# Kernel optimization log

Hardware: AMD Instinct MI355X
Metric: run time of the kernel (lower is better)

Reference implementation:

```python
import jax, jax.numpy as jnp
import numpy as np

N_NODES = 200000
N_EDGES = 6400000
IN_DIM = 15      # pfc_input_dim
POS_DIM = 4      # positional_dim
OUT_DIM = 2      # vtx_classes + 1


def setup_inputs() -> dict:
    key = jax.random.key(0)
    k1, k2, k3, k4, k5, k6, k7 = jax.random.split(key, 7)
    x_pfc = jax.random.normal(k1, (N_NODES, IN_DIM), dtype=jnp.float32)
    edge_index = jax.random.randint(k2, (2, N_EDGES), 0, N_NODES, dtype=jnp.int64)
    s_in = 1.0 / np.sqrt(IN_DIM)
    s_pos = 1.0 / np.sqrt(POS_DIM)
    # PointTransformerConv params: lin, lin_src, lin_dst (no bias), pos_nn = Linear(4, 2)
    W_lin = jax.random.uniform(k3, (OUT_DIM, IN_DIM), jnp.float32, -s_in, s_in)
    W_src = jax.random.uniform(k4, (OUT_DIM, IN_DIM), jnp.float32, -s_in, s_in)
    W_dst = jax.random.uniform(k5, (OUT_DIM, IN_DIM), jnp.float32, -s_in, s_in)
    W_pos = jax.random.uniform(k6, (OUT_DIM, POS_DIM), jnp.float32, -s_pos, s_pos)
    b_pos = jax.random.uniform(k7, (OUT_DIM,), jnp.float32, -s_pos, s_pos)
    return {"x_pfc": x_pfc, "edge_index": edge_index, "W_lin": W_lin,
            "W_src": W_src, "W_dst": W_dst, "W_pos": W_pos, "b_pos": b_pos}


def reference(x_pfc, edge_index, W_lin, W_src, W_dst, W_pos, b_pos):
    n = x_pfc.shape[0]
    pos = x_pfc[:, :POS_DIM]
    # original forward calls ptc_only(x, pos, edge_index.flip(0)):
    # source j = edge_index[1], target i = edge_index[0]
    j = edge_index[1]
    i = edge_index[0]
    # node-level linear maps (N x OUT_DIM)
    v = x_pfc @ W_lin.T
    a_src = x_pfc @ W_src.T
    a_dst = x_pfc @ W_dst.T
    # positional MLP on relative positions (E x OUT_DIM)
    delta = (pos[i] - pos[j]) @ W_pos.T + b_pos
    alpha = a_dst[i] - a_src[j] + delta
    # segment softmax over incoming edges of each target node i
    m = jax.ops.segment_max(alpha, i, num_segments=n)  # -inf for empty segments (never indexed)
    e = jnp.exp(alpha - m[i])
    denom = jax.ops.segment_sum(e, i, num_segments=n)
    attn = e / (denom[i] + 1e-16)
    msg = attn * (v[j] + delta)
    return jax.ops.segment_sum(msg, i, num_segments=n)
```

## Files before the change

### kernel.cpp

```cpp
#include <hip/hip_runtime.h>

#define N_NODES 200000
#define N_EDGES 6400000
#define IN_DIM 15
#define POS_DIM 4

#define CSHIFT 9
#define CMASK 511
#define CW 512
#define NCOARSE ((N_NODES + CW - 1) >> CSHIFT)
#define CHUNK 16384
#define NBLK ((N_EDGES + CHUNK - 1) / CHUNK)
#define CAP 17408
#define SUB 8192

typedef unsigned uv4 __attribute__((ext_vector_type(4)));


__global__ void node_prep(const float* __restrict__ x,
                          const float* __restrict__ Wlin,
                          const float* __restrict__ Wsrc,
                          const float* __restrict__ Wpos,
                          float4* __restrict__ tabJ,
                          unsigned* __restrict__ gcnt)
{
    int n = blockIdx.x * blockDim.x + threadIdx.x;
    if (n < NCOARSE) gcnt[n] = 0u;
    if (n >= N_NODES) return;
    const float* xp = x + (long)n * IN_DIM;
    float xv[IN_DIM];
#pragma unroll
    for (int k = 0; k < IN_DIM; ++k) xv[k] = xp[k];

    float p0 = 0.f, p1 = 0.f;
#pragma unroll
    for (int k = 0; k < POS_DIM; ++k) {
        p0 += Wpos[k] * xv[k];
        p1 += Wpos[POS_DIM + k] * xv[k];
    }
    float v0 = 0.f, v1 = 0.f, as0 = 0.f, as1 = 0.f;
#pragma unroll
    for (int k = 0; k < IN_DIM; ++k) {
        float xk = xv[k];
        v0  += Wlin[k] * xk;  v1  += Wlin[IN_DIM + k] * xk;
        as0 += Wsrc[k] * xk;  as1 += Wsrc[IN_DIM + k] * xk;
    }
    tabJ[n] = make_float4(as0 + p0, as1 + p1, v0 - p0, v1 - p1);
}

__global__ void scatter_kernel(const int* __restrict__ idx,
                               unsigned* __restrict__ gcnt,
                               unsigned* __restrict__ packed)
{
    __shared__ unsigned stage[CHUNK];
    __shared__ unsigned cnt[512];
    __shared__ unsigned sc[512];
    __shared__ unsigned lloc[512];
    __shared__ unsigned gdst[NCOARSE];
    int b = blockIdx.x;
    int t = threadIdx.x;
    long s0 = (long)b * CHUNK;
    int end = (int)min((long)CHUNK, (long)N_EDGES - s0);
    cnt[t] = 0u;
    __syncthreads();
    for (int e = t * 4; e < end; e += 2048) {
        int4 iv = *(const int4*)(idx + s0 + e);
        atomicAdd(&cnt[iv.x >> CSHIFT], 1u);
        atomicAdd(&cnt[iv.y >> CSHIFT], 1u);
        atomicAdd(&cnt[iv.z >> CSHIFT], 1u);
        atomicAdd(&cnt[iv.w >> CSHIFT], 1u);
    }
    __syncthreads();
    sc[t] = cnt[t];
    __syncthreads();
    for (int o = 1; o < 512; o <<= 1) {
        unsigned a = (t >= o) ? sc[t - o] : 0u;
        __syncthreads();
        sc[t] += a;
        __syncthreads();
    }
    {
        unsigned c  = cnt[t];
        unsigned ex = sc[t] - c;
        lloc[t] = ex;
        if (t < NCOARSE) gdst[t] = atomicAdd(&gcnt[t], c);
        cnt[t] = ex;
    }
    __syncthreads();
    for (int e = t * 4; e < end; e += 2048) {
        int4 iv = *(const int4*)(idx + s0 + e);
        int4 jv = *(const int4*)(idx + N_EDGES + s0 + e);
        unsigned r0 = atomicAdd(&cnt[iv.x >> CSHIFT], 1u);
        unsigned r1 = atomicAdd(&cnt[iv.y >> CSHIFT], 1u);
        unsigned r2 = atomicAdd(&cnt[iv.z >> CSHIFT], 1u);
        unsigned r3 = atomicAdd(&cnt[iv.w >> CSHIFT], 1u);
        stage[r0] = ((unsigned)jv.x << CSHIFT) | (unsigned)(iv.x & CMASK);
        stage[r1] = ((unsigned)jv.y << CSHIFT) | (unsigned)(iv.y & CMASK);
        stage[r2] = ((unsigned)jv.z << CSHIFT) | (unsigned)(iv.z & CMASK);
        stage[r3] = ((unsigned)jv.w << CSHIFT) | (unsigned)(iv.w & CMASK);
    }
    __syncthreads();
    int wid = t >> 6, lane = t & 63;
    for (int bk = wid; bk < NCOARSE; bk += 8) {
        unsigned st  = lloc[bk];
        unsigned len = lloc[bk + 1] - st;
        unsigned gb  = gdst[bk];
        unsigned rem = (gb < (unsigned)CAP) ? (unsigned)CAP - gb : 0u;
        if (len > rem) len = rem;
        unsigned* dst = packed + (size_t)bk * CAP + gb;
        for (unsigned e = lane; e < len; e += 64u)
            dst[e] = stage[st + e];
    }
}

__global__ __launch_bounds__(512, 8) void
bucket_agg_kernel(const unsigned* __restrict__ packed,
                  const unsigned* __restrict__ gcnt,
                  const float* __restrict__ x,
                  const float* __restrict__ Wdst,
                  const float* __restrict__ Wpos,
                  const float4* __restrict__ tabJ,
                  const float* __restrict__ bpos,
                  float2* __restrict__ out)
{
    __shared__ unsigned cache[SUB + 512];
    __shared__ unsigned cnt[512], sc[512], cur[512];
    int k = blockIdx.x;
    int t = threadIdx.x;
    float b0 = bpos[0], b1 = bpos[1];
    int gn = (k << CSHIFT) + t;

    float p0 = 0.f, p1 = 0.f, ad0 = 0.f, ad1 = 0.f;
    if (gn < N_NODES) {
        const float* xp = x + (long)gn * IN_DIM;
        float xv[IN_DIM];
#pragma unroll
        for (int q = 0; q < IN_DIM; ++q) xv[q] = xp[q];
#pragma unroll
        for (int q = 0; q < POS_DIM; ++q) {
            p0 += Wpos[q] * xv[q];
            p1 += Wpos[POS_DIM + q] * xv[q];
        }
#pragma unroll
        for (int q = 0; q < IN_DIM; ++q) {
            ad0 += Wdst[q] * xv[q];
            ad1 += Wdst[IN_DIM + q] * xv[q];
        }
    }
    float a0 = ad0 + p0 + b0, a1 = ad1 + p1 + b1;
    float sn0 = 0.f, sn1 = 0.f, sd0 = 0.f, sd1 = 0.f;

    unsigned n = min(gcnt[k], (unsigned)CAP);
    const unsigned* pk = packed + (size_t)k * CAP;

    for (unsigned c0 = 0; c0 < n; c0 += SUB) {
        unsigned m = min(n - c0, (unsigned)SUB);
        cnt[t] = 0u;
        __syncthreads();
        for (unsigned e = 4u * t; e < m; e += 2048u) {
            uv4 p = *(const uv4*)(pk + c0 + e);
            atomicAdd(&cnt[p.x & CMASK], 1u);
            if (e + 1 < m) atomicAdd(&cnt[p.y & CMASK], 1u);
            if (e + 2 < m) atomicAdd(&cnt[p.z & CMASK], 1u);
            if (e + 3 < m) atomicAdd(&cnt[p.w & CMASK], 1u);
        }
        __syncthreads();
        sc[t] = cnt[t];
        __syncthreads();
        for (int o = 1; o < 512; o <<= 1) {
            unsigned a = (t >= o) ? sc[t - o] : 0u;
            __syncthreads();
            sc[t] += a;
            __syncthreads();
        }
        unsigned deg = cnt[t];
        unsigned st  = sc[t] - deg + (unsigned)t;
        cur[t] = st;
        __syncthreads();
        for (unsigned e = 4u * t; e < m; e += 2048u) {
            uv4 p = *(const uv4*)(pk + c0 + e);
            { unsigned pos = atomicAdd(&cur[p.x & CMASK], 1u); cache[pos] = p.x >> CSHIFT; }
            if (e + 1 < m) { unsigned pos = atomicAdd(&cur[p.y & CMASK], 1u); cache[pos] = p.y >> CSHIFT; }
            if (e + 2 < m) { unsigned pos = atomicAdd(&cur[p.z & CMASK], 1u); cache[pos] = p.z >> CSHIFT; }
            if (e + 3 < m) { unsigned pos = atomicAdd(&cur[p.w & CMASK], 1u); cache[pos] = p.w >> CSHIFT; }
        }
        __syncthreads();
        unsigned e = 0;
        for (; e + 4u <= deg; e += 4u) {
            unsigned j0 = cache[st + e],     j1 = cache[st + e + 1];
            unsigned j2 = cache[st + e + 2], j3 = cache[st + e + 3];
            float4 f0 = tabJ[j0], f1 = tabJ[j1], f2 = tabJ[j2], f3 = tabJ[j3];
            float e00 = __expf(a0 - f0.x), e01 = __expf(a1 - f0.y);
            float e10 = __expf(a0 - f1.x), e11 = __expf(a1 - f1.y);
            float e20 = __expf(a0 - f2.x), e21 = __expf(a1 - f2.y);
            float e30 = __expf(a0 - f3.x), e31 = __expf(a1 - f3.y);
            sn0 += e00 * f0.z + e10 * f1.z + e20 * f2.z + e30 * f3.z;
            sn1 += e01 * f0.w + e11 * f1.w + e21 * f2.w + e31 * f3.w;
            sd0 += e00 + e10 + e20 + e30;
            sd1 += e01 + e11 + e21 + e31;
        }
        for (; e < deg; ++e) {
            unsigned j = cache[st + e];
            float4 fj = tabJ[j];
            float e0 = __expf(a0 - fj.x), e1 = __expf(a1 - fj.y);
            sn0 += e0 * fj.z;  sn1 += e1 * fj.w;
            sd0 += e0;         sd1 += e1;
        }
    }

    if (gn >= N_NODES) return;
    float o0 = (sn0 + (p0 + b0) * sd0) / (sd0 + 1e-16f);
    float o1 = (sn1 + (p1 + b1) * sd1) / (sd1 + 1e-16f);
    out[gn] = make_float2(o0, o1);
}

extern "C" void kernel_launch(void* const* d_in, const int* in_sizes, int n_in,
                              void* d_out, int out_size, void* d_ws, size_t ws_size,
                              hipStream_t stream) {
    const float* x    = (const float*)d_in[0];
    const int*   idx  = (const int*)d_in[1];
    const float* Wlin = (const float*)d_in[2];
    const float* Wsrc = (const float*)d_in[3];
    const float* Wdst = (const float*)d_in[4];
    const float* Wpos = (const float*)d_in[5];
    const float* bpos = (const float*)d_in[6];
    float* out = (float*)d_out;

    char* ws = (char*)d_ws;
    size_t off = 0;
    float4* tabJ = (float4*)(ws + off); off += (size_t)N_NODES * 16;
    unsigned* packed = (unsigned*)(ws + off); off += (size_t)NCOARSE * CAP * 4;
    unsigned* gcnt   = (unsigned*)(ws + off); off += (size_t)NCOARSE * 4;

    node_prep<<<(N_NODES + 255) / 256, 256, 0, stream>>>(x, Wlin, Wsrc, Wpos,
                                                         tabJ, gcnt);
    scatter_kernel<<<NBLK, 512, 0, stream>>>(idx, gcnt, packed);
    bucket_agg_kernel<<<NCOARSE, 512, 0, stream>>>(packed, gcnt,
                                                   x, Wdst, Wpos, tabJ, bpos,
                                                   (float2*)out);
}
```

Before: 169.8 us.

## Split each coarse bucket across two blocks and use wave-shuffle scans

The aggregation kernel now launches two 256-thread blocks per 512-node bucket. Each block reads the whole bucket but keeps only edges whose target falls in its half, which removes the SUB-chunk loop and doubles the number of blocks. Both kernels replace the shared-memory Hillis-Steele scan, with its many barriers, by a wave-level shuffle scan plus a small cross-wave sum. The gather loop is unrolled to 8 and the second pass over packed edges uses nontemporal loads. The cost is that every packed edge is read twice from global memory, once per half-block. Per-half capacity HCAP assumes balanced halves, and overflow past HCAP is unchecked.

Measured after the change: 172.6 us. About the same (+1.6%).

```diff
diff --git a/kernel.cpp b/kernel.cpp
--- a/kernel.cpp
+++ b/kernel.cpp
@@ -12,7 +12,7 @@
 #define CHUNK 16384
 #define NBLK ((N_EDGES + CHUNK - 1) / CHUNK)
 #define CAP 17408
-#define SUB 8192
+#define HCAP 8704
 
 typedef unsigned uv4 __attribute__((ext_vector_type(4)));
 
@@ -54,11 +54,12 @@
 {
     __shared__ unsigned stage[CHUNK];
     __shared__ unsigned cnt[512];
-    __shared__ unsigned sc[512];
     __shared__ unsigned lloc[512];
     __shared__ unsigned gdst[NCOARSE];
+    __shared__ unsigned wsum[8];
     int b = blockIdx.x;
     int t = threadIdx.x;
+    int lane = t & 63, wid = t >> 6;
     long s0 = (long)b * CHUNK;
     int end = (int)min((long)CHUNK, (long)N_EDGES - s0);
     cnt[t] = 0u;
@@ -71,20 +72,23 @@
         atomicAdd(&cnt[iv.w >> CSHIFT], 1u);
     }
     __syncthreads();
-    sc[t] = cnt[t];
-    __syncthreads();
-    for (int o = 1; o < 512; o <<= 1) {
-        unsigned a = (t >= o) ? sc[t - o] : 0u;
-        __syncthreads();
-        sc[t] += a;
-        __syncthreads();
-    }
+    unsigned v = cnt[t];
+    unsigned s = v;
+#pragma unroll
+    for (int off = 1; off < 64; off <<= 1) {
+        unsigned u = __shfl_up(s, off, 64);
+        if (lane >= off) s += u;
+    }
+    if (lane == 63) wsum[wid] = s;
+    __syncthreads();
+    unsigned woff = 0;
+#pragma unroll
+    for (int w = 0; w < 8; ++w) woff += (w < wid) ? wsum[w] : 0u;
     {
-        unsigned c  = cnt[t];
-        unsigned ex = sc[t] - c;
+        unsigned ex = woff + s - v;
         lloc[t] = ex;
-        if (t < NCOARSE) gdst[t] = atomicAdd(&gcnt[t], c);
         cnt[t] = ex;
+        if (t < NCOARSE) gdst[t] = atomicAdd(&gcnt[t], v);
     }
     __syncthreads();
     for (int e = t * 4; e < end; e += 2048) {
@@ -100,7 +104,6 @@
         stage[r3] = ((unsigned)jv.w << CSHIFT) | (unsigned)(iv.w & CMASK);
     }
     __syncthreads();
-    int wid = t >> 6, lane = t & 63;
     for (int bk = wid; bk < NCOARSE; bk += 8) {
         unsigned st  = lloc[bk];
         unsigned len = lloc[bk + 1] - st;
@@ -113,7 +116,7 @@
     }
 }
 
-__global__ __launch_bounds__(512, 8) void
+__global__ __launch_bounds__(256) void
 bucket_agg_kernel(const unsigned* __restrict__ packed,
                   const unsigned* __restrict__ gcnt,
                   const float* __restrict__ x,
@@ -123,12 +126,16 @@
                   const float* __restrict__ bpos,
                   float2* __restrict__ out)
 {
-    __shared__ unsigned cache[SUB + 512];
-    __shared__ unsigned cnt[512], sc[512], cur[512];
-    int k = blockIdx.x;
+    __shared__ unsigned cache[HCAP + 512];
+    __shared__ unsigned cnt[256], cur[256];
+    __shared__ unsigned wsum[4];
+    int blk = blockIdx.x;
+    int k = blk >> 1;
+    unsigned half = (unsigned)(blk & 1);
     int t = threadIdx.x;
+    int lane = t & 63, wid = t >> 6;
     float b0 = bpos[0], b1 = bpos[1];
-    int gn = (k << CSHIFT) + t;
+    int gn = (k << CSHIFT) + ((int)half << 8) + t;
 
     float p0 = 0.f, p1 = 0.f, ad0 = 0.f, ad1 = 0.f;
     if (gn < N_NODES) {
@@ -153,59 +160,71 @@
     unsigned n = min(gcnt[k], (unsigned)CAP);
     const unsigned* pk = packed + (size_t)k * CAP;
 
-    for (unsigned c0 = 0; c0 < n; c0 += SUB) {
-        unsigned m = min(n - c0, (unsigned)SUB);
-        cnt[t] = 0u;
-        __syncthreads();
-        for (unsigned e = 4u * t; e < m; e += 2048u) {
-            uv4 p = *(const uv4*)(pk + c0 + e);
-            atomicAdd(&cnt[p.x & CMASK], 1u);
-            if (e + 1 < m) atomicAdd(&cnt[p.y & CMASK], 1u);
-            if (e + 2 < m) atomicAdd(&cnt[p.z & CMASK], 1u);
-            if (e + 3 < m) atomicAdd(&cnt[p.w & CMASK], 1u);
-        }
-        __syncthreads();
-        sc[t] = cnt[t];
-        __syncthreads();
-        for (int o = 1; o < 512; o <<= 1) {
-            unsigned a = (t >= o) ? sc[t - o] : 0u;
-            __syncthreads();
-            sc[t] += a;
-            __syncthreads();
-        }
-        unsigned deg = cnt[t];
-        unsigned st  = sc[t] - deg + (unsigned)t;
-        cur[t] = st;
-        __syncthreads();
-        for (unsigned e = 4u * t; e < m; e += 2048u) {
-            uv4 p = *(const uv4*)(pk + c0 + e);
-            { unsigned pos = atomicAdd(&cur[p.x & CMASK], 1u); cache[pos] = p.x >> CSHIFT; }
-            if (e + 1 < m) { unsigned pos = atomicAdd(&cur[p.y & CMASK], 1u); cache[pos] = p.y >> CSHIFT; }
-            if (e + 2 < m) { unsigned pos = atomicAdd(&cur[p.z & CMASK], 1u); cache[pos] = p.z >> CSHIFT; }
-            if (e + 3 < m) { unsigned pos = atomicAdd(&cur[p.w & CMASK], 1u); cache[pos] = p.w >> CSHIFT; }
-        }
-        __syncthreads();
-        unsigned e = 0;
-        for (; e + 4u <= deg; e += 4u) {
-            unsigned j0 = cache[st + e],     j1 = cache[st + e + 1];
-            unsigned j2 = cache[st + e + 2], j3 = cache[st + e + 3];
-            float4 f0 = tabJ[j0], f1 = tabJ[j1], f2 = tabJ[j2], f3 = tabJ[j3];
-            float e00 = __expf(a0 - f0.x), e01 = __expf(a1 - f0.y);
-            float e10 = __expf(a0 - f1.x), e11 = __expf(a1 - f1.y);
-            float e20 = __expf(a0 - f2.x), e21 = __expf(a1 - f2.y);
-            float e30 = __expf(a0 - f3.x), e31 = __expf(a1 - f3.y);
-            sn0 += e00 * f0.z + e10 * f1.z + e20 * f2.z + e30 * f3.z;
-            sn1 += e01 * f0.w + e11 * f1.w + e21 * f2.w + e31 * f3.w;
-            sd0 += e00 + e10 + e20 + e30;
-            sd1 += e01 + e11 + e21 + e31;
-        }
-        for (; e < deg; ++e) {
-            unsigned j = cache[st + e];
-            float4 fj = tabJ[j];
-            float e0 = __expf(a0 - fj.x), e1 = __expf(a1 - fj.y);
-            sn0 += e0 * fj.z;  sn1 += e1 * fj.w;
-            sd0 += e0;         sd1 += e1;
-        }
+#define KEEP(w) ((((w) & CMASK) >> 8) == half)
+    cnt[t] = 0u;
+    __syncthreads();
+    for (unsigned e = 4u * t; e < n; e += 1024u) {
+        uv4 p = *(const uv4*)(pk + e);
+        if (KEEP(p.x))               atomicAdd(&cnt[p.x & 255u], 1u);
+        if (e + 1 < n && KEEP(p.y))  atomicAdd(&cnt[p.y & 255u], 1u);
+        if (e + 2 < n && KEEP(p.z))  atomicAdd(&cnt[p.z & 255u], 1u);
+        if (e + 3 < n && KEEP(p.w))  atomicAdd(&cnt[p.w & 255u], 1u);
+    }
+    __syncthreads();
+    unsigned v = cnt[t];
+    unsigned s = v;
+#pragma unroll
+    for (int off = 1; off < 64; off <<= 1) {
+        unsigned u = __shfl_up(s, off, 64);
+        if (lane >= off) s += u;
+    }
+    if (lane == 63) wsum[wid] = s;
+    __syncthreads();
+    unsigned woff = 0;
+#pragma unroll
+    for (int w = 0; w < 4; ++w) woff += (w < wid) ? wsum[w] : 0u;
+    unsigned deg = v;
+    unsigned st  = woff + s - v + (unsigned)t;
+    cur[t] = st;
+    __syncthreads();
+    for (unsigned e = 4u * t; e < n; e += 1024u) {
+        uv4 p = __builtin_nontemporal_load((const uv4*)(pk + e));
+        if (KEEP(p.x))              { unsigned pos = atomicAdd(&cur[p.x & 255u], 1u); cache[pos] = p.x >> CSHIFT; }
+        if (e + 1 < n && KEEP(p.y)) { unsigned pos = atomicAdd(&cur[p.y & 255u], 1u); cache[pos] = p.y >> CSHIFT; }
+        if (e + 2 < n && KEEP(p.z)) { unsigned pos = atomicAdd(&cur[p.z & 255u], 1u); cache[pos] = p.z >> CSHIFT; }
+        if (e + 3 < n && KEEP(p.w)) { unsigned pos = atomicAdd(&cur[p.w & 255u], 1u); cache[pos] = p.w >> CSHIFT; }
+    }
+#undef KEEP
+    __syncthreads();
+    unsigned e = 0;
+    for (; e + 8u <= deg; e += 8u) {
+        unsigned j0 = cache[st + e],     j1 = cache[st + e + 1];
+        unsigned j2 = cache[st + e + 2], j3 = cache[st + e + 3];
+        unsigned j4 = cache[st + e + 4], j5 = cache[st + e + 5];
+        unsigned j6 = cache[st + e + 6], j7 = cache[st + e + 7];
+        float4 f0 = tabJ[j0], f1 = tabJ[j1], f2 = tabJ[j2], f3 = tabJ[j3];
+        float4 f4 = tabJ[j4], f5 = tabJ[j5], f6 = tabJ[j6], f7 = tabJ[j7];
+        float e00 = __expf(a0 - f0.x), e01 = __expf(a1 - f0.y);
+        float e10 = __expf(a0 - f1.x), e11 = __expf(a1 - f1.y);
+        float e20 = __expf(a0 - f2.x), e21 = __expf(a1 - f2.y);
+        float e30 = __expf(a0 - f3.x), e31 = __expf(a1 - f3.y);
+        float e40 = __expf(a0 - f4.x), e41 = __expf(a1 - f4.y);
+        float e50 = __expf(a0 - f5.x), e51 = __expf(a1 - f5.y);
+        float e60 = __expf(a0 - f6.x), e61 = __expf(a1 - f6.y);
+        float e70 = __expf(a0 - f7.x), e71 = __expf(a1 - f7.y);
+        sn0 += e00 * f0.z + e10 * f1.z + e20 * f2.z + e30 * f3.z
+             + e40 * f4.z + e50 * f5.z + e60 * f6.z + e70 * f7.z;
+        sn1 += e01 * f0.w + e11 * f1.w + e21 * f2.w + e31 * f3.w
+             + e41 * f4.w + e51 * f5.w + e61 * f6.w + e71 * f7.w;
+        sd0 += e00 + e10 + e20 + e30 + e40 + e50 + e60 + e70;
+        sd1 += e01 + e11 + e21 + e31 + e41 + e51 + e61 + e71;
+    }
+    for (; e < deg; ++e) {
+        unsigned j = cache[st + e];
+        float4 fj = tabJ[j];
+        float e0 = __expf(a0 - fj.x), e1 = __expf(a1 - fj.y);
+        sn0 += e0 * fj.z;  sn1 += e1 * fj.w;
+        sd0 += e0;         sd1 += e1;
     }
 
     if (gn >= N_NODES) return;
@@ -235,7 +254,7 @@
     node_prep<<<(N_NODES + 255) / 256, 256, 0, stream>>>(x, Wlin, Wsrc, Wpos,
                                                          tabJ, gcnt);
     scatter_kernel<<<NBLK, 512, 0, stream>>>(idx, gcnt, packed);
-    bucket_agg_kernel<<<NCOARSE, 512, 0, stream>>>(packed, gcnt,
-                                                   x, Wdst, Wpos, tabJ, bpos,
-                                                   (float2*)out);
-}
+    bucket_agg_kernel<<<NCOARSE * 2, 256, 0, stream>>>(packed, gcnt,
+                                                       x, Wdst, Wpos, tabJ, bpos,
+                                                       (float2*)out);
+}
```
